# Kernel tuning notes

Measured on AMD Instinct MI355X. Metric: run time of the kernel, lower is better.

The kernel has to match this reference:

```python
import jax, jax.numpy as jnp
import numpy as np

N = 100000
E = 1600000
DIN = 165
DH = 128


def setup_inputs() -> dict:
    key = jax.random.key(0)
    ks = jax.random.split(key, 10)
    def nrm(k, shape, scale=0.1):
        return jax.random.normal(k, shape, dtype=jnp.float32) * scale
    x = jax.random.normal(ks[0], (N, DIN), dtype=jnp.float32)
    edge_index = jax.random.randint(ks[1], (2, E), 0, N, dtype=jnp.int64)
    return dict(
        x=x,
        edge_index=edge_index,
        fb_w1=nrm(ks[2], (DIN, DIN // 2)),
        fb_w2=nrm(ks[3], (DIN // 2, DIN)),
        sage_wl=nrm(ks[4], (DIN, DH)),
        sage_bl=jnp.zeros((DH,), jnp.float32),
        sage_wr=nrm(ks[5], (DIN, DH)),
        gat_w=nrm(ks[6], (DH, DH // 2)),
        gat_att_src=nrm(ks[7], (DH // 2,)),
        gat_att_dst=nrm(ks[8], (DH // 2,)),
        gat_b=jnp.zeros((DH // 2,), jnp.float32),
        cheb_w=nrm(ks[9], (DH // 2, 1)),
        cheb_b=jnp.zeros((1,), jnp.float32),
    )


def _segment_softmax(logits, seg, num_segments):
    mx = jax.ops.segment_max(logits, seg, num_segments=num_segments)
    e = jnp.exp(logits - mx[seg])
    s = jax.ops.segment_sum(e, seg, num_segments=num_segments)
    return e / (s[seg] + 1e-16)


def reference(x, edge_index, fb_w1, fb_w2, sage_wl, sage_bl, sage_wr,
              gat_w, gat_att_src, gat_att_dst, gat_b, cheb_w, cheb_b):
    n = x.shape[0]
    src, dst = edge_index[0], edge_index[1]

    # FeatureBooster: scatter over batch=arange(n) is identity for max and sum,
    # so max_result == sum_result == x and y = sigmoid(mlp(x) + mlp(x)).
    m = jnp.maximum(x @ fb_w1, 0.0) @ fb_w2
    x = x * jax.nn.sigmoid(m + m)

    # SAGEConv (mean aggregation): out = lin_l(mean_agg(x_src -> dst)) + lin_r(x)
    agg = jax.ops.segment_sum(x[src], dst, num_segments=n)  # [n, DIN]
    cnt = jax.ops.segment_sum(jnp.ones((src.shape[0],), x.dtype), dst, num_segments=n)
    agg = agg / jnp.maximum(cnt, 1.0)[:, None]
    x = agg @ sage_wl + sage_bl + x @ sage_wr
    x = jnp.maximum(x, 0.0)  # relu; dropout is identity in eval mode

    # GATConv (heads=1) with default add_self_loops=True
    ar = jnp.arange(n, dtype=src.dtype)
    si = jnp.concatenate([src, ar])
    di = jnp.concatenate([dst, ar])
    h = x @ gat_w                      # [n, 64]
    a_s = h @ gat_att_src              # [n]
    a_d = h @ gat_att_dst              # [n]
    e = a_s[si] + a_d[di]
    e = jnp.where(e > 0, e, 0.2 * e)   # leaky_relu slope 0.2
    alpha = _segment_softmax(e, di, n)
    x = jax.ops.segment_sum(h[si] * alpha[:, None], di, num_segments=n) + gat_b
    x = jnp.maximum(x, 0.0)

    # ChebConv with K=1: T_0(x) = x, so it's a plain linear layer.
    x = x @ cheb_w + cheb_b
    return jax.nn.sigmoid(x)
```

## Files before the change

kernel.cpp:

```cpp
#include <hip/hip_runtime.h>
#include <hip/hip_bf16.h>

#define N_NODES 100000
#define N_EDGES 1600000
#define DIN 165
#define DHID 82
#define DH 128
#define DG 64

typedef _Float16 f16;
typedef f16 f16x8 __attribute__((ext_vector_type(8)));
typedef f16 f16x4 __attribute__((ext_vector_type(4)));
typedef f16 f16x2 __attribute__((ext_vector_type(2)));
typedef float f32x4 __attribute__((ext_vector_type(4)));

#define MFMA16(a, b, c) __builtin_amdgcn_mfma_f32_16x16x32_f16(a, b, c, 0, 0, 0)


__global__ __launch_bounds__(256) void rank_xpad_kernel(const float* __restrict__ x,
                                                        f16* __restrict__ Xp,
                                                        const int* __restrict__ dst,
                                                        int* __restrict__ cnt,
                                                        int* __restrict__ rank) {
    int blk = blockIdx.x, tid = threadIdx.x;
    if ((blk & 3) == 0) {
        int e = (blk >> 2) * 256 + tid;
        rank[e] = atomicAdd(&cnt[dst[e]], 1);
    } else {
        int xb = blk - (blk >> 2) - 1;
        int gid = xb * 256 + tid;
        int node = gid / 48, g = gid % 48;
        int col0 = g * 4;
        f16x4 o;
#pragma unroll
        for (int j = 0; j < 4; j++) {
            int c = col0 + j;
            o[j] = (f16)((c < DIN) ? x[(long)node * DIN + c] : 0.f);
        }
        *((f16x4*)(Xp + (long)node * 192 + col0)) = o;
    }
}

__global__ __launch_bounds__(1024) void scan_kernel(const int* __restrict__ cnt,
                                                    int* __restrict__ rowptr,
                                                    int* __restrict__ bsum,
                                                    int* __restrict__ boff,
                                                    int* __restrict__ arrived) {
    __shared__ int wsum[16];
    __shared__ int lastflag;
    int tid = threadIdx.x, lane = tid & 63, wid = tid >> 6;
    int blk = blockIdx.x;
    int i = blk * 1024 + tid;
    int v = (i < N_NODES) ? cnt[i] : 0;
    int xv = v;
#pragma unroll
    for (int off = 1; off < 64; off <<= 1) {
        int t = __shfl_up(xv, off);
        if (lane >= off) xv += t;
    }
    if (lane == 63) wsum[wid] = xv;
    __syncthreads();
    if (wid == 0 && lane < 16) {
        int wv = wsum[lane];
#pragma unroll
        for (int off = 1; off < 16; off <<= 1) {
            int t = __shfl_up(wv, off);
            if (lane >= off) wv += t;
        }
        wsum[lane] = wv;
    }
    __syncthreads();
    int off0 = wid ? wsum[wid - 1] : 0;
    if (i <= N_NODES) rowptr[i] = off0 + xv - v;
    if (tid == 1023) bsum[blk] = off0 + xv;
    __threadfence();
    if (tid == 0) {
        int old = atomicAdd(arrived, 1);
        lastflag = (old == 97);
    }
    __syncthreads();
    if (lastflag && wid == 0) {
        __threadfence();
        int c = 0;
        for (int base = 0; base < 98; base += 64) {
            int idx = base + lane;
            int bv = 0;
            if (idx < 98)
                bv = __hip_atomic_load(&bsum[idx], __ATOMIC_RELAXED,
                                       __HIP_MEMORY_SCOPE_AGENT);
            int sv = bv;
#pragma unroll
            for (int off = 1; off < 64; off <<= 1) {
                int t = __shfl_up(sv, off);
                if (lane >= off) sv += t;
            }
            if (idx < 98) boff[idx] = c + sv - bv;
            c += __shfl(sv, 63);
        }
    }
}

__global__ __launch_bounds__(256) void h_fill_kernel(const f16* __restrict__ Xp,
                                                     const float* __restrict__ w1,
                                                     f16* __restrict__ H,
                                                     const int* __restrict__ src,
                                                     const int* __restrict__ dst,
                                                     const int* __restrict__ rank,
                                                     const int* __restrict__ rowptr,
                                                     const int* __restrict__ boff,
                                                     int* __restrict__ esrc) {
    int tid = threadIdx.x, wave = tid >> 6, lane = tid & 63;
    {
        int tg = blockIdx.x * 256 + tid;
        for (int e = tg; e < N_EDGES; e += 384 * 256) {
            int d = dst[e];
            __builtin_nontemporal_store(src[e], &esrc[rowptr[d] + boff[d >> 10] + rank[e]]);
        }
    }
    int q = lane >> 4, l16 = lane & 15;
    int blk = blockIdx.x;
    int g = (blk >> 3) & 1;
    int chunk = (blk & 7) + 8 * (blk >> 4);
    int nbase = g * 48;
    f16x8 bf[3][6];
#pragma unroll
    for (int nt = 0; nt < 3; nt++) {
        int col = nbase + nt * 16 + l16;
#pragma unroll
        for (int ks = 0; ks < 6; ks++) {
            int kb = ks * 32 + q * 8;
            f16x8 b;
#pragma unroll
            for (int j = 0; j < 8; j++) {
                int k = kb + j;
                b[j] = (f16)((k < DIN && col < DHID) ? w1[k * DHID + col] : 0.f);
            }
            bf[nt][ks] = b;
        }
    }
    for (int mt = chunk * 4 + wave; mt < 6250; mt += 768) {
        const f16* xr = Xp + (long)(mt * 16 + l16) * 192;
        f32x4 acc[3];
#pragma unroll
        for (int nt = 0; nt < 3; nt++) acc[nt] = (f32x4){0.f, 0.f, 0.f, 0.f};
#pragma unroll
        for (int ks = 0; ks < 6; ks++) {
            f16x8 a = *((const f16x8*)(xr + ks * 32 + q * 8));
#pragma unroll
            for (int nt = 0; nt < 3; nt++) acc[nt] = MFMA16(a, bf[nt][ks], acc[nt]);
        }
#pragma unroll
        for (int nt = 0; nt < 3; nt++) {
            int col = nbase + nt * 16 + l16;
#pragma unroll
            for (int r = 0; r < 4; r++) {
                int node = mt * 16 + q * 4 + r;
                H[(long)node * 96 + col] = (f16)fmaxf(acc[nt][r], 0.f);
            }
        }
    }
}

__global__ __launch_bounds__(256) void y_kernel(const f16* __restrict__ Xp,
                                                const f16* __restrict__ H,
                                                const float* __restrict__ w2,
                                                f16* __restrict__ Y) {
    int tid = threadIdx.x, wave = tid >> 6, lane = tid & 63;
    int q = lane >> 4, l16 = lane & 15;
    int blk = blockIdx.x;
    int g = (blk >> 3) & 3;
    int chunk = (blk & 7) + 8 * (blk >> 5);
    int nbase = g * 48;
    f16x8 bf[3][3];
#pragma unroll
    for (int nt = 0; nt < 3; nt++) {
        int col = nbase + nt * 16 + l16;
#pragma unroll
        for (int ks = 0; ks < 3; ks++) {
            int kb = ks * 32 + q * 8;
            f16x8 b;
#pragma unroll
            for (int j = 0; j < 8; j++) {
                int k = kb + j;
                b[j] = (f16)((k < DHID && col < DIN) ? w2[k * DIN + col] : 0.f);
            }
            bf[nt][ks] = b;
        }
    }
    for (int mt = chunk * 4 + wave; mt < 6250; mt += 768) {
        const f16* hr = H + (long)(mt * 16 + l16) * 96;
        f32x4 acc[3];
#pragma unroll
        for (int nt = 0; nt < 3; nt++) acc[nt] = (f32x4){0.f, 0.f, 0.f, 0.f};
#pragma unroll
        for (int ks = 0; ks < 3; ks++) {
            f16x8 a = *((const f16x8*)(hr + ks * 32 + q * 8));
#pragma unroll
            for (int nt = 0; nt < 3; nt++) acc[nt] = MFMA16(a, bf[nt][ks], acc[nt]);
        }
#pragma unroll
        for (int nt = 0; nt < 3; nt++) {
            int col = nbase + nt * 16 + l16;
#pragma unroll
            for (int r = 0; r < 4; r++) {
                int node = mt * 16 + q * 4 + r;
                float gg = 1.f / (1.f + __expf(-2.f * acc[nt][r]));
                float xv = (float)Xp[(long)node * 192 + col];
                Y[(long)node * 192 + col] = (f16)(xv * gg);
            }
        }
    }
}

__global__ __launch_bounds__(256) void sage_lin_kernel(const f16* __restrict__ Y,
                                                       const float* __restrict__ wl,
                                                       const float* __restrict__ wr,
                                                       const float* __restrict__ bl,
                                                       f16* __restrict__ t_l,
                                                       f16* __restrict__ x2) {
    int tid = threadIdx.x, wave = tid >> 6, lane = tid & 63;
    int q = lane >> 4, l16 = lane & 15;
    int blk = blockIdx.x;
    int g = (blk >> 3) & 3;
    int chunk = (blk & 7) + 8 * (blk >> 5);
    bool isR = (g >= 2);
    const float* W = isR ? wr : wl;
    int cbase = (g & 1) * 64;
    f16x8 bf[4][6];
    float blv[4];
#pragma unroll
    for (int nt = 0; nt < 4; nt++) {
        int col = cbase + nt * 16 + l16;
        blv[nt] = isR ? bl[col] : 0.f;
#pragma unroll
        for (int ks = 0; ks < 6; ks++) {
            int kb = ks * 32 + q * 8;
            f16x8 b;
#pragma unroll
            for (int j = 0; j < 8; j++) {
                int k = kb + j;
                b[j] = (f16)((k < DIN) ? W[k * DH + col] : 0.f);
            }
            bf[nt][ks] = b;
        }
    }
    for (int mt = chunk * 4 + wave; mt < 6250; mt += 768) {
        const f16* yrow = Y + (long)(mt * 16 + l16) * 192;
        f32x4 acc[4];
#pragma unroll
        for (int nt = 0; nt < 4; nt++) acc[nt] = (f32x4){0.f, 0.f, 0.f, 0.f};
#pragma unroll
        for (int ks = 0; ks < 6; ks++) {
            f16x8 a = *((const f16x8*)(yrow + ks * 32 + q * 8));
#pragma unroll
            for (int nt = 0; nt < 4; nt++) acc[nt] = MFMA16(a, bf[nt][ks], acc[nt]);
        }
#pragma unroll
        for (int nt = 0; nt < 4; nt++) {
            int col = cbase + nt * 16 + l16;
#pragma unroll
            for (int r = 0; r < 4; r++) {
                int node = mt * 16 + q * 4 + r;
                if (isR)
                    x2[(long)node * DH + col] = (f16)(acc[nt][r] + blv[nt]);
                else
                    t_l[(long)node * DH + col] = (f16)acc[nt][r];
            }
        }
    }
}

__global__ __launch_bounds__(256) void sage_agg_kernel(const f16* __restrict__ t_l,
                                                       const int* __restrict__ rowptr,
                                                       const int* __restrict__ boff,
                                                       const int* __restrict__ esrc,
                                                       f16* __restrict__ x2) {
    int wid = threadIdx.x >> 6, lane = threadIdx.x & 63;
    int i = blockIdx.x * 4 + wid;
    int r0 = rowptr[i] + boff[i >> 10];
    int r1 = rowptr[i + 1] + boff[(i + 1) >> 10];
    int quarter = lane >> 4, fq = lane & 15;
    float acc[8];
#pragma unroll
    for (int k = 0; k < 8; k++) acc[k] = 0.f;
    for (int e0 = r0; e0 < r1; e0 += 64) {
        int cnt = min(64, r1 - e0);
        int sn_v = (lane < cnt) ? esrc[e0 + lane] : 0;
        int jmax = (cnt + 3) >> 2;
        for (int j = 0; j < jmax; j++) {
            int idx = 4 * j + quarter;
            int sn = __shfl(sn_v, idx);
            float v = (idx < cnt) ? 1.f : 0.f;
            f16x8 p = *((const f16x8*)(t_l + ((long)sn << 7) + fq * 8));
#pragma unroll
            for (int k = 0; k < 8; k++) acc[k] = fmaf(v, (float)p[k], acc[k]);
        }
    }
#pragma unroll
    for (int k = 0; k < 8; k++) {
        acc[k] += __shfl_xor(acc[k], 16);
        acc[k] += __shfl_xor(acc[k], 32);
    }
    if (quarter == 0) {
        float inv = 1.f / fmaxf((float)(r1 - r0), 1.f);
        f16x8* xp = (f16x8*)(x2 + (long)i * DH + fq * 8);
        f16x8 pre = *xp;
        f16x8 o;
#pragma unroll
        for (int k = 0; k < 8; k++) o[k] = (f16)fmaxf((float)pre[k] + acc[k] * inv, 0.f);
        *xp = o;
    }
}

__global__ __launch_bounds__(256) void gat_h_kernel(const f16* __restrict__ x2,
                                                    const float* __restrict__ gw,
                                                    const float* __restrict__ att_s_w,
                                                    const float* __restrict__ att_d_w,
                                                    f16* __restrict__ h,
                                                    float* __restrict__ a_s,
                                                    float* __restrict__ a_d) {
    int tid = threadIdx.x, wave = tid >> 6, lane = tid & 63;
    int q = lane >> 4, l16 = lane & 15;
    f16x8 bf[4][4];
    float asw[4], adw[4];
#pragma unroll
    for (int nt = 0; nt < 4; nt++) {
        int col = nt * 16 + l16;
        asw[nt] = att_s_w[col];
        adw[nt] = att_d_w[col];
#pragma unroll
        for (int ks = 0; ks < 4; ks++) {
            int kb = ks * 32 + q * 8;
            f16x8 b;
#pragma unroll
            for (int j = 0; j < 8; j++) b[j] = (f16)gw[(kb + j) * DG + col];
            bf[nt][ks] = b;
        }
    }
    int stride = gridDim.x * 4;
    for (int mt = blockIdx.x * 4 + wave; mt < 6250; mt += stride) {
        const f16* xr = x2 + (long)(mt * 16 + l16) * DH;
        f32x4 acc[4];
#pragma unroll
        for (int nt = 0; nt < 4; nt++) acc[nt] = (f32x4){0.f, 0.f, 0.f, 0.f};
#pragma unroll
        for (int ks = 0; ks < 4; ks++) {
            f16x8 a = *((const f16x8*)(xr + ks * 32 + q * 8));
#pragma unroll
            for (int nt = 0; nt < 4; nt++) acc[nt] = MFMA16(a, bf[nt][ks], acc[nt]);
        }
#pragma unroll
        for (int r = 0; r < 4; r++) {
            int node = mt * 16 + q * 4 + r;
            float vs = 0.f, vd = 0.f;
#pragma unroll
            for (int nt = 0; nt < 4; nt++) {
                float hv = acc[nt][r];
                h[(long)node * DG + nt * 16 + l16] = (f16)hv;
                vs += hv * asw[nt];
                vd += hv * adw[nt];
            }
#pragma unroll
            for (int off = 1; off < 16; off <<= 1) {
                vs += __shfl_xor(vs, off);
                vd += __shfl_xor(vd, off);
            }
            if (l16 == 0) {
                a_s[node] = vs;
                a_d[node] = vd;
            }
        }
    }
}

__device__ __forceinline__ float leaky02(float v) { return v > 0.f ? v : 0.2f * v; }

__global__ __launch_bounds__(256) void gat_agg_kernel(const f16* __restrict__ h,
                                                      const float* __restrict__ a_s,
                                                      const float* __restrict__ a_d,
                                                      const int* __restrict__ rowptr,
                                                      const int* __restrict__ boff,
                                                      const int* __restrict__ esrc,
                                                      const float* __restrict__ gat_b,
                                                      const float* __restrict__ cheb_w,
                                                      const float* __restrict__ cheb_b,
                                                      float* __restrict__ out) {
    int wid = threadIdx.x >> 6, lane = threadIdx.x & 63;
    int i = blockIdx.x * 4 + wid;
    int r0 = rowptr[i] + boff[i >> 10];
    int r1 = rowptr[i + 1] + boff[(i + 1) >> 10];
    int quarter = lane >> 4, fq = lane & 15;
    float adi = a_d[i];
    float acc[4] = {0.f, 0.f, 0.f, 0.f};
    float sv = 0.f;
    for (int e0 = r0; e0 < r1; e0 += 64) {
        int cnt = min(64, r1 - e0);
        int sn_v = (lane < cnt) ? esrc[e0 + lane] : 0;
        float ev = 0.f;
        if (lane < cnt) ev = __expf(leaky02(a_s[sn_v] + adi));
        sv += ev;
        int jmax = (cnt + 3) >> 2;
        for (int j = 0; j < jmax; j++) {
            int idx = 4 * j + quarter;
            int sn = __shfl(sn_v, idx);
            float w = __shfl(ev, idx);
            f16x4 p = *((const f16x4*)(h + ((long)sn << 6) + fq * 4));
#pragma unroll
            for (int k = 0; k < 4; k++) acc[k] = fmaf(w, (float)p[k], acc[k]);
        }
    }
#pragma unroll
    for (int off = 32; off > 0; off >>= 1) sv += __shfl_xor(sv, off);
#pragma unroll
    for (int k = 0; k < 4; k++) {
        acc[k] += __shfl_xor(acc[k], 16);
        acc[k] += __shfl_xor(acc[k], 32);
    }
    if (quarter == 0) {
        float wself = __expf(leaky02(a_s[i] + adi));
        float s = sv + wself;
        f16x4 ph = *((const f16x4*)(h + ((long)i << 6) + fq * 4));
        float4 gb = ((const float4*)gat_b)[fq];
        float4 cw = ((const float4*)cheb_w)[fq];
        float gbv[4] = {gb.x, gb.y, gb.z, gb.w};
        float cwv[4] = {cw.x, cw.y, cw.z, cw.w};
        float inv = 1.f / s;
        float z = 0.f;
#pragma unroll
        for (int k = 0; k < 4; k++) {
            float o = fmaxf(fmaf(wself, (float)ph[k], acc[k]) * inv + gbv[k], 0.f);
            z = fmaf(o, cwv[k], z);
        }
#pragma unroll
        for (int off = 8; off > 0; off >>= 1) z += __shfl_xor(z, off);
        if (fq == 0) out[i] = 1.f / (1.f + __expf(-(z + cheb_b[0])));
    }
}

extern "C" void kernel_launch(void* const* d_in, const int* in_sizes, int n_in,
                              void* d_out, int out_size, void* d_ws, size_t ws_size,
                              hipStream_t stream) {
    const float* x       = (const float*)d_in[0];
    const int*   eidx    = (const int*)d_in[1];
    const float* fb_w1   = (const float*)d_in[2];
    const float* fb_w2   = (const float*)d_in[3];
    const float* sage_wl = (const float*)d_in[4];
    const float* sage_bl = (const float*)d_in[5];
    const float* sage_wr = (const float*)d_in[6];
    const float* gat_w   = (const float*)d_in[7];
    const float* att_src = (const float*)d_in[8];
    const float* att_dst = (const float*)d_in[9];
    const float* gat_b   = (const float*)d_in[10];
    const float* cheb_w  = (const float*)d_in[11];
    const float* cheb_b  = (const float*)d_in[12];

    const int* src = eidx;
    const int* dst = eidx + N_EDGES;

    char* base = (char*)d_ws;
    f16* Xp = (f16*)base;
    f16* H  = (f16*)(base + 38400000);
    f16* Y  = (f16*)(base + 57600000);
    f16* t_l = (f16*)base;
    f16* x2  = (f16*)(base + 25600000);
    f16* h   = Y;
    float* a_s = (float*)(base + 70400000);
    float* a_d = a_s + N_NODES;
    int* rowptr  = (int*)(base + 96000000);
    int* cnt     = rowptr + (N_NODES + 1);
    int* arrived = cnt + N_NODES;
    int* esrc    = arrived + 1;
    int* rank    = esrc + N_EDGES;
    int* bsum    = rank + N_EDGES;
    int* boff    = bsum + 128;

    hipMemsetAsync(cnt, 0, (N_NODES + 1) * sizeof(int), stream);

    rank_xpad_kernel<<<25000, 256, 0, stream>>>(x, Xp, dst, cnt, rank);
    scan_kernel<<<98, 1024, 0, stream>>>(cnt, rowptr, bsum, boff, arrived);
    h_fill_kernel<<<384, 256, 0, stream>>>(Xp, fb_w1, H, src, dst, rank, rowptr, boff, esrc);
    y_kernel<<<768, 256, 0, stream>>>(Xp, H, fb_w2, Y);
    sage_lin_kernel<<<768, 256, 0, stream>>>(Y, sage_wl, sage_wr, sage_bl, t_l, x2);
    sage_agg_kernel<<<N_NODES / 4, 256, 0, stream>>>(t_l, rowptr, boff, esrc, x2);
    gat_h_kernel<<<392, 256, 0, stream>>>(x2, gat_w, att_src, att_dst, h, a_s, a_d);
    gat_agg_kernel<<<N_NODES / 4, 256, 0, stream>>>(h, a_s, a_d, rowptr, boff, esrc, gat_b,
                                                    cheb_w, cheb_b, (float*)d_out);
}
```

Baseline: 492.1 us.

## Regroup kernel fusion: pair edge ranking with H GEMM, fill with Y GEMM

Splits the x padding into its own kernel, then fuses the atomic edge-rank counting with the first FeatureBooster GEMM (H) in one launch. The esrc CSR fill moves into the Y GEMM kernel. The aim is to overlap latency-bound atomics and scatter stores with MFMA work and to cut one dependent launch stage. The cost is an extra launch for xpad, and the H GEMM now runs in only about 1042 blocks interleaved with the rank blocks.

```diff
diff --git a/kernel.cpp b/kernel.cpp
--- a/kernel.cpp
+++ b/kernel.cpp
@@ -17,27 +17,76 @@
 #define MFMA16(a, b, c) __builtin_amdgcn_mfma_f32_16x16x32_f16(a, b, c, 0, 0, 0)
 
 
-__global__ __launch_bounds__(256) void rank_xpad_kernel(const float* __restrict__ x,
-                                                        f16* __restrict__ Xp,
-                                                        const int* __restrict__ dst,
-                                                        int* __restrict__ cnt,
-                                                        int* __restrict__ rank) {
+__global__ __launch_bounds__(256) void xpad_kernel(const float* __restrict__ x,
+                                                   f16* __restrict__ Xp) {
+    int gid = blockIdx.x * 256 + threadIdx.x;
+    int node = gid / 48, g = gid % 48;
+    int col0 = g * 4;
+    f16x4 o;
+#pragma unroll
+    for (int j = 0; j < 4; j++) {
+        int c = col0 + j;
+        o[j] = (f16)((c < DIN) ? x[(long)node * DIN + c] : 0.f);
+    }
+    *((f16x4*)(Xp + (long)node * 192 + col0)) = o;
+}
+
+__global__ __launch_bounds__(256) void rank_h_kernel(const int* __restrict__ dst,
+                                                     int* __restrict__ cnt,
+                                                     int* __restrict__ rank,
+                                                     const f16* __restrict__ Xp,
+                                                     const float* __restrict__ w1,
+                                                     f16* __restrict__ H) {
     int blk = blockIdx.x, tid = threadIdx.x;
-    if ((blk & 3) == 0) {
-        int e = (blk >> 2) * 256 + tid;
-        rank[e] = atomicAdd(&cnt[dst[e]], 1);
-    } else {
-        int xb = blk - (blk >> 2) - 1;
-        int gid = xb * 256 + tid;
-        int node = gid / 48, g = gid % 48;
-        int col0 = g * 4;
-        f16x4 o;
-#pragma unroll
-        for (int j = 0; j < 4; j++) {
-            int c = col0 + j;
-            o[j] = (f16)((c < DIN) ? x[(long)node * DIN + c] : 0.f);
-        }
-        *((f16x4*)(Xp + (long)node * 192 + col0)) = o;
+    if ((blk & 3) != 3) {
+        int rb = 3 * (blk >> 2) + (blk & 3);
+        if (rb < 6250) {
+            int e = rb * 256 + tid;
+            rank[e] = atomicAdd(&cnt[dst[e]], 1);
+        }
+        return;
+    }
+    int hb = blk >> 2;
+    int wave = tid >> 6, lane = tid & 63;
+    int q = lane >> 4, l16 = lane & 15;
+    int g = hb & 1;
+    int nbase = g * 48;
+    f16x8 bf[3][6];
+#pragma unroll
+    for (int nt = 0; nt < 3; nt++) {
+        int col = nbase + nt * 16 + l16;
+#pragma unroll
+        for (int ks = 0; ks < 6; ks++) {
+            int kb = ks * 32 + q * 8;
+            f16x8 b;
+#pragma unroll
+            for (int j = 0; j < 8; j++) {
+                int k = kb + j;
+                b[j] = (f16)((k < DIN && col < DHID) ? w1[k * DHID + col] : 0.f);
+            }
+            bf[nt][ks] = b;
+        }
+    }
+    for (int mt = (hb >> 1) * 4 + wave; mt < 6250; mt += 1042 * 4) {
+        const f16* xr = Xp + (long)(mt * 16 + l16) * 192;
+        f32x4 acc[3];
+#pragma unroll
+        for (int nt = 0; nt < 3; nt++) acc[nt] = (f32x4){0.f, 0.f, 0.f, 0.f};
+#pragma unroll
+        for (int ks = 0; ks < 6; ks++) {
+            f16x8 a = *((const f16x8*)(xr + ks * 32 + q * 8));
+#pragma unroll
+            for (int nt = 0; nt < 3; nt++) acc[nt] = MFMA16(a, bf[nt][ks], acc[nt]);
+        }
+#pragma unroll
+        for (int nt = 0; nt < 3; nt++) {
+            int col = nbase + nt * 16 + l16;
+#pragma unroll
+            for (int r = 0; r < 4; r++) {
+                int node = mt * 16 + q * 4 + r;
+                H[(long)node * 96 + col] = (f16)fmaxf(acc[nt][r], 0.f);
+            }
+        }
     }
 }
 
@@ -100,9 +149,10 @@
     }
 }
 
-__global__ __launch_bounds__(256) void h_fill_kernel(const f16* __restrict__ Xp,
-                                                     const float* __restrict__ w1,
-                                                     f16* __restrict__ H,
+__global__ __launch_bounds__(256) void y_fill_kernel(const f16* __restrict__ Xp,
+                                                     const f16* __restrict__ H,
+                                                     const float* __restrict__ w2,
+                                                     f16* __restrict__ Y,
                                                      const int* __restrict__ src,
                                                      const int* __restrict__ dst,
                                                      const int* __restrict__ rank,
@@ -112,60 +162,11 @@
     int tid = threadIdx.x, wave = tid >> 6, lane = tid & 63;
     {
         int tg = blockIdx.x * 256 + tid;
-        for (int e = tg; e < N_EDGES; e += 384 * 256) {
+        for (int e = tg; e < N_EDGES; e += 768 * 256) {
             int d = dst[e];
             __builtin_nontemporal_store(src[e], &esrc[rowptr[d] + boff[d >> 10] + rank[e]]);
         }
     }
-    int q = lane >> 4, l16 = lane & 15;
-    int blk = blockIdx.x;
-    int g = (blk >> 3) & 1;
-    int chunk = (blk & 7) + 8 * (blk >> 4);
-    int nbase = g * 48;
-    f16x8 bf[3][6];
-#pragma unroll
-    for (int nt = 0; nt < 3; nt++) {
-        int col = nbase + nt * 16 + l16;
-#pragma unroll
-        for (int ks = 0; ks < 6; ks++) {
-            int kb = ks * 32 + q * 8;
-            f16x8 b;
-#pragma unroll
-            for (int j = 0; j < 8; j++) {
-                int k = kb + j;
-                b[j] = (f16)((k < DIN && col < DHID) ? w1[k * DHID + col] : 0.f);
-            }
-            bf[nt][ks] = b;
-        }
-    }
-    for (int mt = chunk * 4 + wave; mt < 6250; mt += 768) {
-        const f16* xr = Xp + (long)(mt * 16 + l16) * 192;
-        f32x4 acc[3];
-#pragma unroll
-        for (int nt = 0; nt < 3; nt++) acc[nt] = (f32x4){0.f, 0.f, 0.f, 0.f};
-#pragma unroll
-        for (int ks = 0; ks < 6; ks++) {
-            f16x8 a = *((const f16x8*)(xr + ks * 32 + q * 8));
-#pragma unroll
-            for (int nt = 0; nt < 3; nt++) acc[nt] = MFMA16(a, bf[nt][ks], acc[nt]);
-        }
-#pragma unroll
-        for (int nt = 0; nt < 3; nt++) {
-            int col = nbase + nt * 16 + l16;
-#pragma unroll
-            for (int r = 0; r < 4; r++) {
-                int node = mt * 16 + q * 4 + r;
-                H[(long)node * 96 + col] = (f16)fmaxf(acc[nt][r], 0.f);
-            }
-        }
-    }
-}
-
-__global__ __launch_bounds__(256) void y_kernel(const f16* __restrict__ Xp,
-                                                const f16* __restrict__ H,
-                                                const float* __restrict__ w2,
-                                                f16* __restrict__ Y) {
-    int tid = threadIdx.x, wave = tid >> 6, lane = tid & 63;
     int q = lane >> 4, l16 = lane & 15;
     int blk = blockIdx.x;
     int g = (blk >> 3) & 3;
@@ -476,10 +477,11 @@
 
     hipMemsetAsync(cnt, 0, (N_NODES + 1) * sizeof(int), stream);
 
-    rank_xpad_kernel<<<25000, 256, 0, stream>>>(x, Xp, dst, cnt, rank);
+    xpad_kernel<<<(N_NODES * 48) / 256, 256, 0, stream>>>(x, Xp);
+    rank_h_kernel<<<8336, 256, 0, stream>>>(dst, cnt, rank, Xp, fb_w1, H);
     scan_kernel<<<98, 1024, 0, stream>>>(cnt, rowptr, bsum, boff, arrived);
-    h_fill_kernel<<<384, 256, 0, stream>>>(Xp, fb_w1, H, src, dst, rank, rowptr, boff, esrc);
-    y_kernel<<<768, 256, 0, stream>>>(Xp, H, fb_w2, Y);
+    y_fill_kernel<<<768, 256, 0, stream>>>(Xp, H, fb_w2, Y, src, dst, rank, rowptr, boff,
+                                           esrc);
     sage_lin_kernel<<<768, 256, 0, stream>>>(Y, sage_wl, sage_wr, sage_bl, t_l, x2);
     sage_agg_kernel<<<N_NODES / 4, 256, 0, stream>>>(t_l, rowptr, boff, esrc, x2);
     gat_h_kernel<<<392, 256, 0, stream>>>(x2, gat_w, att_src, att_dst, h, a_s, a_d);
```

New measurement: 598.3 us. 1.22x slower.
